# Kernel tuning notes

Hardware: AMD Instinct MI355X
Metric: run time of the kernel (lower is better)

Reference implementation:

```python
import jax, jax.numpy as jnp
import numpy as np

N, H, W, M = 1, 128, 128, 8
IN_CH, STYLE, VDIR, MASK, HID = 64, 128, 3, 680, 256


def setup_inputs() -> dict:
    key = jax.random.key(0)
    ks = iter(jax.random.split(key, 48))

    def rn(shape, scale=1.0):
        return jax.random.normal(next(ks), shape, jnp.float32) * scale

    d = {}
    d["x"] = rn((N, H, W, M, IN_CH))
    d["raydir"] = rn((N, H, W, 1, VDIR))
    d["z"] = rn((N, STYLE))
    d["m"] = jax.random.uniform(next(ks), (N, H, W, M, MASK), jnp.float32)
    d["fc_m_a_w"] = rn((HID, MASK), 1.0 / np.sqrt(MASK))
    d["fc_viewdir_w"] = rn((HID, VDIR), 1.0 / np.sqrt(VDIR))
    d["fc1_w"] = rn((HID, IN_CH), 1.0 / np.sqrt(IN_CH))
    d["fc1_b"] = jnp.zeros((HID,), jnp.float32)
    for name in ["fc2", "fc3", "fc4", "fc6"]:
        d[name + "_w"] = rn((HID, HID), 1.0 / np.sqrt(HID))
        d[name + "_wa"] = rn((HID, STYLE), 1.0 / np.sqrt(STYLE))
        d[name + "_ba"] = jnp.ones((HID,), jnp.float32)
        d[name + "_wb"] = rn((HID, STYLE), 1.0 / np.sqrt(STYLE))
        d[name + "_bb"] = jnp.zeros((HID,), jnp.float32)
    d["fc_sigma_w"] = rn((1, HID), 1.0 / np.sqrt(HID))
    d["fc_sigma_b"] = jnp.zeros((1,), jnp.float32)
    d["fc5_w"] = rn((HID, HID), 1.0 / np.sqrt(HID))
    d["mod5_wa"] = rn((HID, STYLE), 1.0 / np.sqrt(STYLE))
    d["mod5_ba"] = jnp.ones((HID,), jnp.float32)
    d["mod5_wb"] = rn((HID, STYLE), 1.0 / np.sqrt(STYLE))
    d["mod5_bb"] = jnp.zeros((HID,), jnp.float32)
    d["fc_out_c_w"] = rn((3, HID), 1.0 / np.sqrt(HID))
    d["fc_out_c_b"] = jnp.zeros((3,), jnp.float32)
    return d


def _act(v):
    # LeakyReLU(0.2)
    return jnp.where(v >= 0, v, 0.2 * v)


def _modlin(f, z, w, wa, ba, wb, bb):
    # ModLinear with bias=False, mod_bias=True, output_mode=True.
    # Torch materializes per-sample modulated weights w*alpha then baddbmm;
    # mathematically identical to scaling the input: y = (f*alpha) @ w.T + beta.
    alpha = z @ wa.T + ba  # (N, in)
    beta = z @ wb.T + bb   # (N, out)
    y = jnp.einsum('bhwmi,oi->bhwmo', f * alpha[:, None, None, None, :], w)
    return y + beta[:, None, None, None, :]


def reference(x, raydir, z, m, fc_m_a_w, fc_viewdir_w, fc1_w, fc1_b,
              fc2_w, fc2_wa, fc2_ba, fc2_wb, fc2_bb,
              fc3_w, fc3_wa, fc3_ba, fc3_wb, fc3_bb,
              fc4_w, fc4_wa, fc4_ba, fc4_wb, fc4_bb,
              fc_sigma_w, fc_sigma_b, fc5_w,
              mod5_wa, mod5_ba, mod5_wb, mod5_bb,
              fc6_w, fc6_wa, fc6_ba, fc6_wb, fc6_bb,
              fc_out_c_w, fc_out_c_b):
    f = jnp.einsum('bhwmi,oi->bhwmo', x, fc1_w) + fc1_b
    f = f + jnp.einsum('bhwmi,oi->bhwmo', m, fc_m_a_w)  # use_seg branch
    f = _act(f)
    f = _act(_modlin(f, z, fc2_w, fc2_wa, fc2_ba, fc2_wb, fc2_bb))
    f = _act(_modlin(f, z, fc3_w, fc3_wa, fc3_ba, fc3_wb, fc3_bb))
    f = _act(_modlin(f, z, fc4_w, fc4_wa, fc4_ba, fc4_wb, fc4_bb))
    sigma = jnp.einsum('bhwmi,oi->bhwmo', f, fc_sigma_w) + fc_sigma_b
    # viewdir branch: plain linear, add view-direction features, AffineMod
    f = jnp.einsum('bhwmi,oi->bhwmo', f, fc5_w)
    f = f + jnp.einsum('bhwvi,oi->bhwvo', raydir, fc_viewdir_w)  # broadcasts over M
    alpha5 = z @ mod5_wa.T + mod5_ba
    beta5 = z @ mod5_wb.T + mod5_bb
    f = _act(f * alpha5[:, None, None, None, :] + beta5[:, None, None, None, :])
    f = _act(_modlin(f, z, fc6_w, fc6_wa, fc6_ba, fc6_wb, fc6_bb))
    c = jnp.einsum('bhwmi,oi->bhwmo', f, fc_out_c_w) + fc_out_c_b
    return (sigma, c)
```

## Files before the change

kernel.cpp:

```cpp
#include <hip/hip_runtime.h>

#define US unsigned short

typedef short bf16x8 __attribute__((ext_vector_type(8)));
typedef float f32x4 __attribute__((ext_vector_type(4)));

__device__ __forceinline__ float b2f(US u) {
  union { unsigned u; float f; } x; x.u = ((unsigned)u) << 16; return x.f;
}
__device__ __forceinline__ US f2b(float f) {
  union { float f; unsigned u; } x; x.f = f;
  unsigned r = x.u + 0x7FFFu + ((x.u >> 16) & 1u);
  return (US)(r >> 16);
}
__device__ __forceinline__ float lk(float v) { return v >= 0.f ? v : 0.2f * v; }

__device__ __forceinline__ float ldin(const void* p, int i, int fl) {
  return fl ? ((const float*)p)[i] : b2f(((const US*)p)[i]);
}

#define O_W1 0
#define O_W2 393216
#define O_W3 524288
#define O_W4 655360
#define O_W5 786432
#define O_W6 917504
#define O_B2 1048576
#define O_B3 1049600
#define O_B4 1050624
#define O_B6 1051648
#define O_VD 1052672
#define O_A2 1056800
#define O_A3 1057824
#define O_A4 1058848
#define O_A6 1059872
#define O_A5 1060896
#define O_B5 1061920
#define O_FLAG 1062944

__global__ void detect_dtype(const void* x, char* ws) {
  if (threadIdx.x == 0) {
    const US* p = (const US*)x;
    int wild = 0;
    for (int i = 0; i < 512; ++i) {
      float v = b2f(p[i]);
      float a = fabsf(v);
      if (!(a <= 1e3f) || (a != 0.f && a < 1e-3f)) ++wild;
    }
    *(int*)(ws + O_FLAG) = (wild > 32) ? 1 : 0;
  }
}

struct S1Args {
  const void* z;
  const void* w[10];
  const void* b[10];
};

__global__ void setup_vec(S1Args a, char* ws) {
  const int outoff[10] = {O_A2, O_A3, O_A4, O_A6, O_B2, O_B3, O_B4, O_B6, O_A5, O_B5};
  int fl = *(const int*)(ws + O_FLAG);
  int v = blockIdx.x, k = threadIdx.x;
  const void* W = a.w[v];
  float acc = ldin(a.b[v], k, fl);
  for (int s = 0; s < 128; ++s) acc += ldin(a.z, s, fl) * ldin(W, k * 128 + s, fl);
  *(float*)(ws + outoff[v] + k * 4) = acc;
}

struct S2Args {
  const void *fc1_w, *fc1_b, *m_w, *w2, *w3, *w4, *w5, *w6, *vdw;
};

__global__ void setup_w(S2Args a, char* ws) {
  int fl = *(const int*)(ws + O_FLAG);
  int b = blockIdx.x, t = threadIdx.x;
  if (b < 256) {
    int n = b;
    US* W1p = (US*)(ws + O_W1);
    for (int i = 0; i < 3; ++i) {
      int k = t + i * 256;
      float v;
      if (k < 64) v = ldin(a.fc1_w, n * 64 + k, fl);
      else if (k < 744) v = ldin(a.m_w, n * 680 + k - 64, fl);
      else if (k == 744) v = ldin(a.fc1_b, n, fl);
      else v = 0.f;
      W1p[n * 768 + k] = f2b(v);
    }
  } else if (b < 1536) {
    int li = (b - 256) >> 8;
    int n = (b - 256) & 255;
    int k = t;
    const void* Wsrc = (li == 0) ? a.w2 : (li == 1) ? a.w3 : (li == 2) ? a.w4
                      : (li == 3) ? a.w5 : a.w6;
    const int aoff[5] = {O_A2, O_A3, O_A4, O_A5, O_A6};
    US* Wdst = (US*)(ws + O_W2 + li * 131072);
    float alpha = (li == 3) ? *(const float*)(ws + O_A5 + n * 4)
                            : *(const float*)(ws + aoff[li] + k * 4);
    Wdst[n * 256 + k] = f2b(ldin(Wsrc, n * 256 + k, fl) * alpha);
  } else {
    int n = t;
    float a5 = *(const float*)(ws + O_A5 + n * 4);
    float b5 = *(const float*)(ws + O_B5 + n * 4);
    float* vp = (float*)(ws + O_VD + n * 16);
    vp[0] = a5 * ldin(a.vdw, n * 3 + 0, fl);
    vp[1] = a5 * ldin(a.vdw, n * 3 + 1, fl);
    vp[2] = a5 * ldin(a.vdw, n * 3 + 2, fl);
    vp[3] = b5;
  }
}

__global__ __launch_bounds__(512, 2) void mlp_main(
    const void* __restrict__ x, const void* __restrict__ rdir, const void* __restrict__ m,
    const void* __restrict__ wsig, const void* __restrict__ bsig,
    const void* __restrict__ wout, const void* __restrict__ bout,
    const char* __restrict__ ws, void* __restrict__ out) {
  __shared__ US lds[81920];
  const int fl = *(const int*)(ws + O_FLAG);
  const int tid = threadIdx.x;
  const int wave = tid >> 6, lane = tid & 63;
  const int l16 = lane & 15, q = lane >> 4;
  const int wr = wave & 3;
  const int wcg = wave >> 2;
  const int R0 = blockIdx.x * 256;

  const US* W1p = (const US*)(ws + O_W1);
  const US* W2p = (const US*)(ws + O_W2);
  const US* W3p = (const US*)(ws + O_W3);
  const US* W4p = (const US*)(ws + O_W4);
  const US* W5p = (const US*)(ws + O_W5);
  const US* W6p = (const US*)(ws + O_W6);

  f32x4 acc[4][8];

  const int srow = lane >> 2, skk = (lane & 3) * 8;

  auto loadW = [&](const US* W, int KS, int s, bf16x8 v[2]) {
#pragma unroll
    for (int it = 0; it < 2; ++it) {
      int n = (wave * 2 + it) * 16 + srow;
      v[it] = *(const bf16x8*)(W + n * KS + s * 32 + skk);
    }
  };
  auto storeW = [&](int buf, const bf16x8 v[2]) {
#pragma unroll
    for (int it = 0; it < 2; ++it)
      *(bf16x8*)&lds[65536 + buf * 8192 + (wave * 2 + it) * 512 + lane * 8] = v[it];
  };
  auto loadXM = [&](int s, bf16x8 v[2]) {
#pragma unroll
    for (int it = 0; it < 2; ++it) {
      int g = R0 + (wave * 2 + it) * 16 + srow;
      const void* base = nullptr;
      int off = 0;
      if (s < 2) { base = x; off = g * 64 + s * 32 + skk; }
      else if (s < 23) { base = m; off = g * 680 + (s * 32 - 64) + skk; }
      else if (skk == 0) { base = m; off = g * 680 + 672; }
      if (base) {
        if (fl) {
          const float* p = (const float*)base + off;
          bf16x8 t;
#pragma unroll
          for (int j = 0; j < 8; ++j) t[j] = (short)f2b(p[j]);
          v[it] = t;
        } else {
          v[it] = *(const bf16x8*)((const US*)base + off);
        }
      } else {
        bf16x8 t = {0, 0, 0, 0, 0, 0, 0, 0};
        if (skk == 8) t[0] = (short)0x3F80;
        v[it] = t;
      }
    }
  };
  auto storeXM = [&](int buf, const bf16x8 v[2]) {
#pragma unroll
    for (int it = 0; it < 2; ++it)
      *(bf16x8*)&lds[buf * 8192 + (wave * 2 + it) * 512 + lane * 8] = v[it];
  };

  auto computeStep = [&](int s, int buf, bool fromXM) {
    bf16x8 a[4];
    if (fromXM) {
#pragma unroll
      for (int rt = 0; rt < 4; ++rt) {
        int r = wr * 64 + rt * 16 + l16;
        a[rt] = *(const bf16x8*)&lds[buf * 8192 + r * 32 + q * 8];
      }
    } else {
#pragma unroll
      for (int rt = 0; rt < 4; ++rt) {
        int r = wr * 64 + rt * 16 + l16;
        a[rt] = *(const bf16x8*)&lds[r * 256 + ((((s << 2) + q) ^ (r & 7)) << 3)];
      }
    }
    int wbase = 65536 + buf * 8192 + (wcg * 128 + l16) * 32 + q * 8;
#pragma unroll
    for (int nt = 0; nt < 8; ++nt) {
      bf16x8 b = *(const bf16x8*)&lds[wbase + nt * 512];
#pragma unroll
      for (int rt = 0; rt < 4; ++rt)
        acc[rt][nt] = __builtin_amdgcn_mfma_f32_16x16x32_bf16(a[rt], b, acc[rt][nt], 0, 0, 0);
    }
  };
  auto initZero = [&]() {
    f32x4 z = {0.f, 0.f, 0.f, 0.f};
#pragma unroll
    for (int rt = 0; rt < 4; ++rt)
#pragma unroll
      for (int nt = 0; nt < 8; ++nt) acc[rt][nt] = z;
  };
  auto initBeta = [&](int off) {
#pragma unroll
    for (int nt = 0; nt < 8; ++nt) {
      float bv = *(const float*)(ws + off + (wcg * 128 + nt * 16 + l16) * 4);
      f32x4 t = {bv, bv, bv, bv};
#pragma unroll
      for (int rt = 0; rt < 4; ++rt) acc[rt][nt] = t;
    }
  };
  auto runLayer = [&](const US* W) {
    bf16x8 v[2];
    loadW(W, 256, 0, v);
    storeW(0, v);
#pragma unroll 1
    for (int s = 0; s < 8; ++s) {
      bf16x8 nv[2];
      if (s < 7) loadW(W, 256, s + 1, nv);
      __syncthreads();
      computeStep(s, s & 1, false);
      if (s < 7) storeW((s + 1) & 1, nv);
    }
    __syncthreads();
  };
  auto epiAct = [&]() {
#pragma unroll
    for (int nt = 0; nt < 8; ++nt) {
      int k = wcg * 128 + nt * 16 + l16;
#pragma unroll
      for (int rt = 0; rt < 4; ++rt) {
#pragma unroll
        for (int rg = 0; rg < 4; ++rg) {
          int r = wr * 64 + rt * 16 + q * 4 + rg;
          lds[r * 256 + ((((k >> 3) ^ (r & 7))) << 3) + (k & 7)] = f2b(lk(acc[rt][nt][rg]));
        }
      }
    }
    __syncthreads();
  };

  initZero();
  {
    bf16x8 vw[2], va[2];
    loadW(W1p, 768, 0, vw);
    loadXM(0, va);
    storeW(0, vw);
    storeXM(0, va);
#pragma unroll 1
    for (int s = 0; s < 24; ++s) {
      bf16x8 nw[2], na[2];
      if (s < 23) { loadW(W1p, 768, s + 1, nw); loadXM(s + 1, na); }
      __syncthreads();
      computeStep(s, s & 1, true);
      if (s < 23) { storeW((s + 1) & 1, nw); storeXM((s + 1) & 1, na); }
    }
    __syncthreads();
  }
  epiAct();

  initBeta(O_B2); runLayer(W2p); epiAct();
  initBeta(O_B3); runLayer(W3p); epiAct();
  initBeta(O_B4); runLayer(W4p); epiAct();

  {
    int r = tid >> 1, hf = tid & 1, g = R0 + r;
    float sg = 0.f;
#pragma unroll
    for (int cc = 0; cc < 16; ++cc) {
      int ch = hf * 16 + cc;
      bf16x8 av = *(const bf16x8*)&lds[r * 256 + ((ch ^ (r & 7)) << 3)];
#pragma unroll
      for (int j = 0; j < 8; ++j) sg += b2f((US)av[j]) * ldin(wsig, ch * 8 + j, fl);
    }
    sg += __shfl_xor(sg, 1);
    if (!hf) {
      float v = sg + ldin(bsig, 0, fl);
      if (fl) ((float*)out)[g] = v; else ((US*)out)[g] = f2b(v);
    }
  }

  initZero();
  runLayer(W5p);
  if (tid < 96) ((float*)&lds[65536])[tid] = ldin(rdir, (R0 >> 3) * 3 + tid, fl);
  __syncthreads();
  {
    const float* rays = (const float*)&lds[65536];
    float ry[4][3];
#pragma unroll
    for (int rt = 0; rt < 4; ++rt) {
      int p = wr * 8 + rt * 2 + (q >> 1);
      ry[rt][0] = rays[p * 3 + 0]; ry[rt][1] = rays[p * 3 + 1]; ry[rt][2] = rays[p * 3 + 2];
    }
#pragma unroll
    for (int nt = 0; nt < 8; ++nt) {
      int n = wcg * 128 + nt * 16 + l16;
      float4 vp = *(const float4*)(ws + O_VD + n * 16);
#pragma unroll
      for (int rt = 0; rt < 4; ++rt) {
#pragma unroll
        for (int rg = 0; rg < 4; ++rg) {
          float v = acc[rt][nt][rg] + ry[rt][0] * vp.x + ry[rt][1] * vp.y + ry[rt][2] * vp.z + vp.w;
          v = lk(v);
          int r = wr * 64 + rt * 16 + q * 4 + rg;
          lds[r * 256 + ((((n >> 3) ^ (r & 7))) << 3) + (n & 7)] = f2b(v);
        }
      }
    }
  }
  __syncthreads();

  initBeta(O_B6); runLayer(W6p); epiAct();

  {
    int r = tid >> 1, hf = tid & 1, g = R0 + r;
    float c0 = 0.f, c1 = 0.f, c2 = 0.f;
#pragma unroll
    for (int cc = 0; cc < 16; ++cc) {
      int ch = hf * 16 + cc;
      bf16x8 av = *(const bf16x8*)&lds[r * 256 + ((ch ^ (r & 7)) << 3)];
#pragma unroll
      for (int j = 0; j < 8; ++j) {
        float f = b2f((US)av[j]);
        int ci = ch * 8 + j;
        c0 += f * ldin(wout, ci, fl);
        c1 += f * ldin(wout, 256 + ci, fl);
        c2 += f * ldin(wout, 512 + ci, fl);
      }
    }
    c0 += __shfl_xor(c0, 1); c1 += __shfl_xor(c1, 1); c2 += __shfl_xor(c2, 1);
    if (!hf) {
      float v0 = c0 + ldin(bout, 0, fl);
      float v1 = c1 + ldin(bout, 1, fl);
      float v2 = c2 + ldin(bout, 2, fl);
      if (fl) {
        float* o = (float*)out + 131072 + g * 3;
        o[0] = v0; o[1] = v1; o[2] = v2;
      } else {
        US* o = (US*)out + 131072 + g * 3;
        o[0] = f2b(v0); o[1] = f2b(v1); o[2] = f2b(v2);
      }
    }
  }
}

extern "C" void kernel_launch(void* const* d_in, const int* in_sizes, int n_in,
                              void* d_out, int out_size, void* d_ws, size_t ws_size,
                              hipStream_t stream) {
  const void* in[37];
  for (int i = 0; i < 37 && i < n_in; ++i) in[i] = d_in[i];
  char* ws = (char*)d_ws;

  detect_dtype<<<1, 64, 0, stream>>>(in[0], ws);

  S1Args a1;
  a1.z = in[2];
  const int wi[10] = {9, 14, 19, 24, 11, 16, 21, 26, 31, 33};
  const int bi[10] = {10, 15, 20, 25, 12, 17, 22, 27, 32, 34};
  for (int i = 0; i < 10; ++i) { a1.w[i] = in[wi[i]]; a1.b[i] = in[bi[i]]; }
  setup_vec<<<10, 256, 0, stream>>>(a1, ws);

  S2Args a2{in[6], in[7], in[4], in[8], in[13], in[18], in[30], in[23], in[5]};
  setup_w<<<1537, 256, 0, stream>>>(a2, ws);

  mlp_main<<<512, 512, 0, stream>>>(in[0], in[1], in[3], in[28], in[29], in[35], in[36],
                                    (const char*)ws, d_out);
}
```

Before: 1.096 ms.

## Shrink row tile to 64 and read weights directly from global/L2

Each block now handles 64 rows with 4 waves instead of 256 rows with 8 waves, and launches four times as many blocks. Weight B-fragments are loaded straight from global memory (L2-resident) instead of being staged through LDS, which removes the per-k-step weight staging and most barriers in the hidden layers. LDS drops to 40KB so more blocks fit per CU. In exchange each weight element is fetched four times as often, so weight traffic from L2 grows and MFMA feeds now wait on global-load latency.

```diff
diff --git a/kernel.cpp b/kernel.cpp
--- a/kernel.cpp
+++ b/kernel.cpp
@@ -109,19 +109,77 @@
   }
 }
 
-__global__ __launch_bounds__(512, 2) void mlp_main(
+
+#define FACT(r, c) (((r) << 8) + ((((c) ^ ((r) & 7))) << 3))
+#define STG(buf, r, c) (16384 + ((buf) << 11) + ((r) << 5) + ((((c) ^ ((r) & 3))) << 3))
+
+#define INITZERO() do { f32x4 zz = {0.f, 0.f, 0.f, 0.f};                      \
+  _Pragma("unroll") for (int rt = 0; rt < 4; ++rt)                            \
+  _Pragma("unroll") for (int nt = 0; nt < 4; ++nt) acc[rt][nt] = zz; } while (0)
+
+#define INITBETA(OFF) do {                                                    \
+  _Pragma("unroll") for (int nt = 0; nt < 4; ++nt) {                          \
+    float bv = *(const float*)(ws + (OFF) + ((wave << 6) + (nt << 4) + l16) * 4); \
+    f32x4 tt = {bv, bv, bv, bv};                                              \
+    _Pragma("unroll") for (int rt = 0; rt < 4; ++rt) acc[rt][nt] = tt; } } while (0)
+
+#define LAYER256(WP) do {                                                     \
+  _Pragma("unroll 4") for (int ks = 0; ks < 8; ++ks) {                        \
+    bf16x8 a[4];                                                              \
+    _Pragma("unroll") for (int rt = 0; rt < 4; ++rt) {                        \
+      int r = (rt << 4) + l16;                                                \
+      a[rt] = *(const bf16x8*)&lds[FACT(r, (ks << 2) + q)];                   \
+    }                                                                         \
+    _Pragma("unroll") for (int nt = 0; nt < 4; ++nt) {                        \
+      bf16x8 b = *(const bf16x8*)((WP) + ((wave << 6) + (nt << 4) + l16) * 256 + (ks << 5) + (q << 3)); \
+      _Pragma("unroll") for (int rt = 0; rt < 4; ++rt)                        \
+        acc[rt][nt] = __builtin_amdgcn_mfma_f32_16x16x32_bf16(a[rt], b, acc[rt][nt], 0, 0, 0); \
+    }                                                                         \
+  } } while (0)
+
+#define EPIACT() do {                                                         \
+  _Pragma("unroll") for (int nt = 0; nt < 4; ++nt) {                          \
+    int k = (wave << 6) + (nt << 4) + l16;                                    \
+    _Pragma("unroll") for (int rt = 0; rt < 4; ++rt)                          \
+    _Pragma("unroll") for (int rg = 0; rg < 4; ++rg) {                        \
+      int r = (rt << 4) + (q << 2) + rg;                                      \
+      lds[FACT(r, k >> 3) + (k & 7)] = f2b(lk(acc[rt][nt][rg]));              \
+    } }                                                                       \
+  __syncthreads(); } while (0)
+
+__device__ __forceinline__ bf16x8 loadA1(const void* __restrict__ x,
+                                         const void* __restrict__ m,
+                                         int fl, int g, int s, int skk) {
+  int k = s * 32 + skk;
+  bf16x8 v = {0, 0, 0, 0, 0, 0, 0, 0};
+  if (k < 744) {
+    if (fl) {
+      const float* p = (k < 64) ? (const float*)x + g * 64 + k
+                                : (const float*)m + g * 680 + (k - 64);
+#pragma unroll
+      for (int j = 0; j < 8; ++j) v[j] = (short)f2b(p[j]);
+    } else {
+      const US* p = (k < 64) ? (const US*)x + g * 64 + k
+                             : (const US*)m + g * 680 + (k - 64);
+      v = *(const bf16x8*)p;
+    }
+  } else if (k == 744) {
+    v[0] = (short)0x3F80;
+  }
+  return v;
+}
+
+__global__ __launch_bounds__(256, 2) void mlp_main(
     const void* __restrict__ x, const void* __restrict__ rdir, const void* __restrict__ m,
     const void* __restrict__ wsig, const void* __restrict__ bsig,
     const void* __restrict__ wout, const void* __restrict__ bout,
     const char* __restrict__ ws, void* __restrict__ out) {
-  __shared__ US lds[81920];
+  __shared__ US lds[20480];
   const int fl = *(const int*)(ws + O_FLAG);
   const int tid = threadIdx.x;
   const int wave = tid >> 6, lane = tid & 63;
   const int l16 = lane & 15, q = lane >> 4;
-  const int wr = wave & 3;
-  const int wcg = wave >> 2;
-  const int R0 = blockIdx.x * 256;
+  const int R0 = blockIdx.x * 64;
 
   const US* W1p = (const US*)(ws + O_W1);
   const US* W2p = (const US*)(ws + O_W2);
@@ -130,179 +188,73 @@
   const US* W5p = (const US*)(ws + O_W5);
   const US* W6p = (const US*)(ws + O_W6);
 
-  f32x4 acc[4][8];
-
-  const int srow = lane >> 2, skk = (lane & 3) * 8;
-
-  auto loadW = [&](const US* W, int KS, int s, bf16x8 v[2]) {
-#pragma unroll
-    for (int it = 0; it < 2; ++it) {
-      int n = (wave * 2 + it) * 16 + srow;
-      v[it] = *(const bf16x8*)(W + n * KS + s * 32 + skk);
-    }
-  };
-  auto storeW = [&](int buf, const bf16x8 v[2]) {
-#pragma unroll
-    for (int it = 0; it < 2; ++it)
-      *(bf16x8*)&lds[65536 + buf * 8192 + (wave * 2 + it) * 512 + lane * 8] = v[it];
-  };
-  auto loadXM = [&](int s, bf16x8 v[2]) {
-#pragma unroll
-    for (int it = 0; it < 2; ++it) {
-      int g = R0 + (wave * 2 + it) * 16 + srow;
-      const void* base = nullptr;
-      int off = 0;
-      if (s < 2) { base = x; off = g * 64 + s * 32 + skk; }
-      else if (s < 23) { base = m; off = g * 680 + (s * 32 - 64) + skk; }
-      else if (skk == 0) { base = m; off = g * 680 + 672; }
-      if (base) {
-        if (fl) {
-          const float* p = (const float*)base + off;
-          bf16x8 t;
-#pragma unroll
-          for (int j = 0; j < 8; ++j) t[j] = (short)f2b(p[j]);
-          v[it] = t;
-        } else {
-          v[it] = *(const bf16x8*)((const US*)base + off);
-        }
-      } else {
-        bf16x8 t = {0, 0, 0, 0, 0, 0, 0, 0};
-        if (skk == 8) t[0] = (short)0x3F80;
-        v[it] = t;
-      }
-    }
-  };
-  auto storeXM = [&](int buf, const bf16x8 v[2]) {
-#pragma unroll
-    for (int it = 0; it < 2; ++it)
-      *(bf16x8*)&lds[buf * 8192 + (wave * 2 + it) * 512 + lane * 8] = v[it];
-  };
-
-  auto computeStep = [&](int s, int buf, bool fromXM) {
-    bf16x8 a[4];
-    if (fromXM) {
-#pragma unroll
-      for (int rt = 0; rt < 4; ++rt) {
-        int r = wr * 64 + rt * 16 + l16;
-        a[rt] = *(const bf16x8*)&lds[buf * 8192 + r * 32 + q * 8];
-      }
-    } else {
-#pragma unroll
-      for (int rt = 0; rt < 4; ++rt) {
-        int r = wr * 64 + rt * 16 + l16;
-        a[rt] = *(const bf16x8*)&lds[r * 256 + ((((s << 2) + q) ^ (r & 7)) << 3)];
-      }
-    }
-    int wbase = 65536 + buf * 8192 + (wcg * 128 + l16) * 32 + q * 8;
-#pragma unroll
-    for (int nt = 0; nt < 8; ++nt) {
-      bf16x8 b = *(const bf16x8*)&lds[wbase + nt * 512];
-#pragma unroll
-      for (int rt = 0; rt < 4; ++rt)
-        acc[rt][nt] = __builtin_amdgcn_mfma_f32_16x16x32_bf16(a[rt], b, acc[rt][nt], 0, 0, 0);
-    }
-  };
-  auto initZero = [&]() {
-    f32x4 z = {0.f, 0.f, 0.f, 0.f};
-#pragma unroll
-    for (int rt = 0; rt < 4; ++rt)
-#pragma unroll
-      for (int nt = 0; nt < 8; ++nt) acc[rt][nt] = z;
-  };
-  auto initBeta = [&](int off) {
-#pragma unroll
-    for (int nt = 0; nt < 8; ++nt) {
-      float bv = *(const float*)(ws + off + (wcg * 128 + nt * 16 + l16) * 4);
-      f32x4 t = {bv, bv, bv, bv};
-#pragma unroll
-      for (int rt = 0; rt < 4; ++rt) acc[rt][nt] = t;
-    }
-  };
-  auto runLayer = [&](const US* W) {
-    bf16x8 v[2];
-    loadW(W, 256, 0, v);
-    storeW(0, v);
-#pragma unroll 1
-    for (int s = 0; s < 8; ++s) {
-      bf16x8 nv[2];
-      if (s < 7) loadW(W, 256, s + 1, nv);
-      __syncthreads();
-      computeStep(s, s & 1, false);
-      if (s < 7) storeW((s + 1) & 1, nv);
-    }
-    __syncthreads();
-  };
-  auto epiAct = [&]() {
-#pragma unroll
-    for (int nt = 0; nt < 8; ++nt) {
-      int k = wcg * 128 + nt * 16 + l16;
-#pragma unroll
-      for (int rt = 0; rt < 4; ++rt) {
-#pragma unroll
-        for (int rg = 0; rg < 4; ++rg) {
-          int r = wr * 64 + rt * 16 + q * 4 + rg;
-          lds[r * 256 + ((((k >> 3) ^ (r & 7))) << 3) + (k & 7)] = f2b(lk(acc[rt][nt][rg]));
-        }
-      }
-    }
-    __syncthreads();
-  };
-
-  initZero();
+  f32x4 acc[4][4];
+
+  INITZERO();
   {
-    bf16x8 vw[2], va[2];
-    loadW(W1p, 768, 0, vw);
-    loadXM(0, va);
-    storeW(0, vw);
-    storeXM(0, va);
+    const int srow = tid >> 2, skk = (tid & 3) << 3, g = R0 + srow;
+    bf16x8 cur = loadA1(x, m, fl, g, 0, skk);
+    *(bf16x8*)&lds[STG(0, srow, skk >> 3)] = cur;
 #pragma unroll 1
     for (int s = 0; s < 24; ++s) {
-      bf16x8 nw[2], na[2];
-      if (s < 23) { loadW(W1p, 768, s + 1, nw); loadXM(s + 1, na); }
+      bf16x8 nxt;
+      if (s < 23) nxt = loadA1(x, m, fl, g, s + 1, skk);
       __syncthreads();
-      computeStep(s, s & 1, true);
-      if (s < 23) { storeW((s + 1) & 1, nw); storeXM((s + 1) & 1, na); }
-    }
-    __syncthreads();
-  }
-  epiAct();
-
-  initBeta(O_B2); runLayer(W2p); epiAct();
-  initBeta(O_B3); runLayer(W3p); epiAct();
-  initBeta(O_B4); runLayer(W4p); epiAct();
+      bf16x8 a[4];
+#pragma unroll
+      for (int rt = 0; rt < 4; ++rt) {
+        int r = (rt << 4) + l16;
+        a[rt] = *(const bf16x8*)&lds[STG(s & 1, r, q)];
+      }
+#pragma unroll
+      for (int nt = 0; nt < 4; ++nt) {
+        bf16x8 b = *(const bf16x8*)(W1p + ((wave << 6) + (nt << 4) + l16) * 768 + (s << 5) + (q << 3));
+#pragma unroll
+        for (int rt = 0; rt < 4; ++rt)
+          acc[rt][nt] = __builtin_amdgcn_mfma_f32_16x16x32_bf16(a[rt], b, acc[rt][nt], 0, 0, 0);
+      }
+      if (s < 23) *(bf16x8*)&lds[STG((s + 1) & 1, srow, skk >> 3)] = nxt;
+    }
+  }
+  EPIACT();
+
+  INITBETA(O_B2); LAYER256(W2p); __syncthreads(); EPIACT();
+  INITBETA(O_B3); LAYER256(W3p); __syncthreads(); EPIACT();
+  INITBETA(O_B4); LAYER256(W4p); __syncthreads(); EPIACT();
 
   {
-    int r = tid >> 1, hf = tid & 1, g = R0 + r;
-    float sg = 0.f;
-#pragma unroll
-    for (int cc = 0; cc < 16; ++cc) {
-      int ch = hf * 16 + cc;
-      bf16x8 av = *(const bf16x8*)&lds[r * 256 + ((ch ^ (r & 7)) << 3)];
-#pragma unroll
-      for (int j = 0; j < 8; ++j) sg += b2f((US)av[j]) * ldin(wsig, ch * 8 + j, fl);
-    }
-    sg += __shfl_xor(sg, 1);
-    if (!hf) {
-      float v = sg + ldin(bsig, 0, fl);
+    int r = tid >> 2, q4 = tid & 3, g = R0 + r;
+    float sgv = 0.f;
+#pragma unroll
+    for (int i = 0; i < 8; ++i) {
+      int c = q4 * 8 + i;
+      bf16x8 av = *(const bf16x8*)&lds[FACT(r, c)];
+#pragma unroll
+      for (int j = 0; j < 8; ++j) sgv += b2f((US)av[j]) * ldin(wsig, c * 8 + j, fl);
+    }
+    sgv += __shfl_xor(sgv, 1);
+    sgv += __shfl_xor(sgv, 2);
+    if (q4 == 0) {
+      float v = sgv + ldin(bsig, 0, fl);
       if (fl) ((float*)out)[g] = v; else ((US*)out)[g] = f2b(v);
     }
   }
-
-  initZero();
-  runLayer(W5p);
-  if (tid < 96) ((float*)&lds[65536])[tid] = ldin(rdir, (R0 >> 3) * 3 + tid, fl);
+  if (tid < 24) ((float*)&lds[16384])[tid] = ldin(rdir, (R0 >> 3) * 3 + tid, fl);
+
+  INITZERO();
+  LAYER256(W5p);
   __syncthreads();
   {
-    const float* rays = (const float*)&lds[65536];
+    const float* rays = (const float*)&lds[16384];
     float ry[4][3];
 #pragma unroll
     for (int rt = 0; rt < 4; ++rt) {
-      int p = wr * 8 + rt * 2 + (q >> 1);
+      int p = rt * 2 + (q >> 1);
       ry[rt][0] = rays[p * 3 + 0]; ry[rt][1] = rays[p * 3 + 1]; ry[rt][2] = rays[p * 3 + 2];
     }
 #pragma unroll
-    for (int nt = 0; nt < 8; ++nt) {
-      int n = wcg * 128 + nt * 16 + l16;
+    for (int nt = 0; nt < 4; ++nt) {
+      int n = (wave << 6) + (nt << 4) + l16;
       float4 vp = *(const float4*)(ws + O_VD + n * 16);
 #pragma unroll
       for (int rt = 0; rt < 4; ++rt) {
@@ -310,34 +262,36 @@
         for (int rg = 0; rg < 4; ++rg) {
           float v = acc[rt][nt][rg] + ry[rt][0] * vp.x + ry[rt][1] * vp.y + ry[rt][2] * vp.z + vp.w;
           v = lk(v);
-          int r = wr * 64 + rt * 16 + q * 4 + rg;
-          lds[r * 256 + ((((n >> 3) ^ (r & 7))) << 3) + (n & 7)] = f2b(v);
+          int r = (rt << 4) + (q << 2) + rg;
+          lds[FACT(r, n >> 3) + (n & 7)] = f2b(v);
         }
       }
     }
   }
   __syncthreads();
 
-  initBeta(O_B6); runLayer(W6p); epiAct();
+  INITBETA(O_B6); LAYER256(W6p); __syncthreads(); EPIACT();
 
   {
-    int r = tid >> 1, hf = tid & 1, g = R0 + r;
+    int r = tid >> 2, q4 = tid & 3, g = R0 + r;
     float c0 = 0.f, c1 = 0.f, c2 = 0.f;
 #pragma unroll
-    for (int cc = 0; cc < 16; ++cc) {
-      int ch = hf * 16 + cc;
-      bf16x8 av = *(const bf16x8*)&lds[r * 256 + ((ch ^ (r & 7)) << 3)];
+    for (int i = 0; i < 8; ++i) {
+      int c = q4 * 8 + i;
+      bf16x8 av = *(const bf16x8*)&lds[FACT(r, c)];
 #pragma unroll
       for (int j = 0; j < 8; ++j) {
         float f = b2f((US)av[j]);
-        int ci = ch * 8 + j;
+        int ci = c * 8 + j;
         c0 += f * ldin(wout, ci, fl);
         c1 += f * ldin(wout, 256 + ci, fl);
         c2 += f * ldin(wout, 512 + ci, fl);
       }
     }
-    c0 += __shfl_xor(c0, 1); c1 += __shfl_xor(c1, 1); c2 += __shfl_xor(c2, 1);
-    if (!hf) {
+    c0 += __shfl_xor(c0, 1); c0 += __shfl_xor(c0, 2);
+    c1 += __shfl_xor(c1, 1); c1 += __shfl_xor(c1, 2);
+    c2 += __shfl_xor(c2, 1); c2 += __shfl_xor(c2, 2);
+    if (q4 == 0) {
       float v0 = c0 + ldin(bout, 0, fl);
       float v1 = c1 + ldin(bout, 1, fl);
       float v2 = c2 + ldin(bout, 2, fl);
@@ -371,6 +325,6 @@
   S2Args a2{in[6], in[7], in[4], in[8], in[13], in[18], in[30], in[23], in[5]};
   setup_w<<<1537, 256, 0, stream>>>(a2, ws);
 
-  mlp_main<<<512, 512, 0, stream>>>(in[0], in[1], in[3], in[28], in[29], in[35], in[36],
-                                    (const char*)ws, d_out);
-}
+  mlp_main<<<2048, 256, 0, stream>>>(in[0], in[1], in[3], in[28], in[29], in[35], in[36],
+                                     (const char*)ws, d_out);
+}
```

New measurement: 885.4 us. -19.2%, faster.
